# Kernel optimization log

Hardware: AMD Instinct MI355X
Metric: run time of the kernel (lower is better)

The kernel has to match this reference:

```python
import jax, jax.numpy as jnp
import numpy as np
import math

N_HEADS = 16  # matches init_kwargs n_heads


def setup_inputs() -> dict:
    key = jax.random.key(0)
    k1, k2, k3 = jax.random.split(key, 3)
    B, S, D = 8, 1024, 1024
    x = jax.random.normal(k1, (B, S, D), dtype=jnp.float32)
    Wc = jax.random.normal(k2, (D, 3 * D), dtype=jnp.float32) * 0.02
    bc = jnp.zeros((3 * D,), dtype=jnp.float32)
    Wo = jax.random.normal(k3, (D, D), dtype=jnp.float32) * 0.02
    bo = jnp.zeros((D,), dtype=jnp.float32)
    return {"x": x, "Wc": Wc, "bc": bc, "Wo": Wo, "bo": bo}


def reference(x, Wc, bc, Wo, bo):
    B, S, D = x.shape
    H = N_HEADS
    hd = D // H
    qkv = x @ Wc + bc                         # [B,S,3D]
    q, k, v = jnp.split(qkv, 3, axis=2)
    q = q.reshape(B, S, H, hd)
    k = k.reshape(B, S, H, hd)
    v = v.reshape(B, S, H, hd)
    # NOTE: source scales by sqrt(d_size), not sqrt(head_dim)
    scores = jnp.einsum("bqhd,bkhd->bhqk", q, k) / math.sqrt(D)
    # source mask: triu(ones) kept, zeros (k < q) filled with float32 min
    # i.e. attend only to positions k >= q (anti-causal, faithful to source)
    keep = jnp.triu(jnp.ones((S, S), dtype=bool))  # [S,S]
    neg = jnp.finfo(jnp.float32).min
    scores = jnp.where(keep[None, None, :, :], scores, neg)
    attn = jax.nn.softmax(scores, axis=-1)    # [B,H,S,S]; dropout p=0 -> identity
    out = jnp.einsum("bhqk,bkhd->bqhd", attn, v)
    concat = out.reshape(B, S, D)
    return concat @ Wo + bo                   # final dropout p=0 -> identity
```

## Files before the change

kernel.cpp:

```cpp
#include <hip/hip_runtime.h>
#include <stdint.h>

typedef __attribute__((ext_vector_type(8))) short  bf16x8;
typedef __attribute__((ext_vector_type(4))) short  short4v;
typedef __attribute__((ext_vector_type(4))) float  f32x4;
typedef __attribute__((ext_vector_type(4))) float  float4v;

#define VMW(N) asm volatile("s_waitcnt vmcnt(" #N ")" ::: "memory")
#define BAR()  asm volatile("s_barrier" ::: "memory")

__device__ __forceinline__ short f2bf(float f) {
  union { float f; uint32_t u; } c; c.f = f;
  uint32_t u = c.u;
  uint32_t r = (u + 0x7FFFu + ((u >> 16) & 1u)) >> 16;
  return (short)(uint16_t)r;
}

__device__ __forceinline__ short f2bf_hw(float f) {
  return __builtin_bit_cast(short, (__bf16)f);
}

__device__ __forceinline__ void gload_lds16(const void* g, void* l) {
  __builtin_amdgcn_global_load_lds(
      (const __attribute__((address_space(1))) void*)g,
      (__attribute__((address_space(3))) void*)l, 16, 0, 0);
}

__device__ __forceinline__ void transpose_body(
    const float* __restrict__ in, short* __restrict__ out, int R, int C,
    int bx, int by, short (*tile)[65]) {
  int bc = bx * 64, br = by * 64;
  int tc = threadIdx.x & 63, tr = threadIdx.x >> 6;
#pragma unroll
  for (int i = 0; i < 64; i += 4)
    tile[tc][tr + i] = f2bf(in[(size_t)(br + tr + i) * C + bc + tc]);
  __syncthreads();
#pragma unroll
  for (int i = 0; i < 64; i += 4)
    out[(size_t)(bc + tr + i) * R + br + tc] = tile[tr + i][tc];
}

__global__ __launch_bounds__(256) void k_prep(
    const float* __restrict__ x, short* __restrict__ xb, int n4,
    const float* __restrict__ Wc, short* __restrict__ wct,
    const float* __restrict__ Wo, short* __restrict__ wot) {
  __shared__ short tile[64][65];
  const int id = blockIdx.x;
  if (id < 1024) {
    const int stride = 1024 * 256;
    for (int i = id * 256 + threadIdx.x; i < n4; i += stride) {
      float4v v = *(const float4v*)(x + (size_t)i * 4);
      short4v o;
      o.x = f2bf(v.x); o.y = f2bf(v.y); o.z = f2bf(v.z); o.w = f2bf(v.w);
      *(short4v*)(xb + (size_t)i * 4) = o;
    }
  } else if (id < 1024 + 768) {
    int t = id - 1024;
    transpose_body(Wc, wct, 1024, 3072, t % 48, t / 48, tile);
  } else {
    int t = id - 1792;
    transpose_body(Wo, wot, 1024, 1024, t & 15, t >> 4, tile);
  }
}

template <bool F32OUT>
__global__ __launch_bounds__(256) void k_gemm2(
    const short* __restrict__ A, const short* __restrict__ BT,
    const float* __restrict__ bias, void* __restrict__ Cout,
    int M, int N, int K, int nbn) {
  __shared__ short SM[2][2][2][128][32];
  const int tid = threadIdx.x;
  const int w = tid >> 6, l = tid & 63;
  const int fr = l & 15, fg = l >> 4;
  const int wm = w >> 1, wn = w & 1;

  const int q8 = gridDim.x >> 3;
  const int wg = (blockIdx.x & 7) * q8 + (blockIdx.x >> 3);
  const int bm = wg / nbn, bn = wg % nbn;
  const size_t brow = (size_t)bm << 7;
  const int bcol = bn << 7;

  const int NT = K >> 6;

  const int srow = l >> 2;
  const int soct = (l & 3) ^ ((l >> 3) & 3);
  const short* aG = A + (brow + srow) * (size_t)K + soct * 8;
  const short* bG = BT + ((size_t)(bcol + srow)) * K + soct * 8;
  const int slot8 = ((fg ^ ((fr >> 1) & 3)) << 3);

  f32x4 acc[4][4] = {};

#pragma unroll
  for (int s = 0; s < 6; ++s) {
    const int t = s >> 2, tau = s & 3, buf = t & 1, mat = tau & 1, kh = tau >> 1;
    const int kbase = t * 64 + kh * 32;
    const short* g0 = (mat ? bG : aG) + kbase;
#pragma unroll
    for (int j = 0; j < 2; ++j) {
      const int r0 = (w * 2 + j) * 16;
      gload_lds16(g0 + (size_t)r0 * K, (char*)&SM[buf][mat][kh][r0][0]);
    }
  }
  VMW(8);
  BAR();

  int sidx = 6;
  for (int t = 0; t < NT; ++t) {
    const int buf = t & 1;
#pragma unroll
    for (int p = 0; p < 2; ++p) {
      const int kh = p;
#pragma unroll
      for (int s = 0; s < 2; ++s) {
        if (sidx < NT * 4) {
          const int ts = sidx >> 2, tau = sidx & 3;
          const int sb = ts & 1, mat = tau & 1, skh = tau >> 1;
          const int kbase = ts * 64 + skh * 32;
          const short* g0 = (mat ? bG : aG) + kbase;
#pragma unroll
          for (int j = 0; j < 2; ++j) {
            const int r0 = (w * 2 + j) * 16;
            gload_lds16(g0 + (size_t)r0 * K, (char*)&SM[sb][mat][skh][r0][0]);
          }
          ++sidx;
        }
      }
      bf16x8 af[4], bf[4];
#pragma unroll
      for (int m = 0; m < 4; ++m)
        af[m] = *(const bf16x8*)&SM[buf][0][kh][wm * 64 + m * 16 + fr][slot8];
#pragma unroll
      for (int n = 0; n < 4; ++n)
        bf[n] = *(const bf16x8*)&SM[buf][1][kh][wn * 64 + n * 16 + fr][slot8];
      BAR();
      __builtin_amdgcn_s_setprio(1);
#pragma unroll
      for (int m = 0; m < 4; ++m)
#pragma unroll
        for (int n = 0; n < 4; ++n)
          acc[m][n] = __builtin_amdgcn_mfma_f32_16x16x32_bf16(
              af[m], bf[n], acc[m][n], 0, 0, 0);
      __builtin_amdgcn_s_setprio(0);
      if (!(t == NT - 1 && p == 1)) {
        if (t == NT - 1 && p == 0) { VMW(0); }
        else if (t == NT - 2 && p == 1) { VMW(4); }
        else { VMW(8); }
        BAR();
      }
    }
  }

#pragma unroll
  for (int n = 0; n < 4; ++n) {
    const int col = bcol + wn * 64 + n * 16 + fr;
    const float bv = bias[col];
#pragma unroll
    for (int i = 0; i < 4; ++i) {
      const size_t row = brow + (size_t)(wm * 64 + i * 16 + fg * 4);
#pragma unroll
      for (int r = 0; r < 4; ++r) {
        const float v = acc[i][n][r] + bv;
        if (F32OUT)
          ((float*)Cout)[(row + r) * (size_t)N + col] = v;
        else
          ((short*)Cout)[(row + r) * (size_t)N + col] = f2bf(v);
      }
    }
  }
}

__global__ __launch_bounds__(256) void k_attn(
    const short* __restrict__ qkv, short* __restrict__ outc, int Bn, int S) {
  __shared__ short Ks[64][64];
  __shared__ short Vt[64][72];

  const int tid = threadIdx.x;
  const int w = tid >> 6, l = tid & 63;
  const int fr = l & 15, fg = l >> 4;

  const int tq = blockIdx.x >> 7;
  const int bh = blockIdx.x & 127;
  const int h = bh & 15, b = bh >> 4;
  const int q0 = tq << 6;

  const size_t rowbase = (size_t)b * S;
  const int qcol = q0 + w * 16 + fr;

  bf16x8 qf[2];
  {
    const short* qp = qkv + (rowbase + qcol) * 3072 + h * 64 + fg * 8;
    qf[0] = *(const bf16x8*)qp;
    qf[1] = *(const bf16x8*)(qp + 32);
    const float C2 = 0.04508422f;
#pragma unroll
    for (int j = 0; j < 8; ++j) {
      union { float f; uint32_t u; } ca, cb;
      ca.u = ((uint32_t)(uint16_t)qf[0][j]) << 16;
      cb.u = ((uint32_t)(uint16_t)qf[1][j]) << 16;
      qf[0][j] = f2bf_hw(ca.f * C2);
      qf[1][j] = f2bf_hw(cb.f * C2);
    }
  }

  f32x4 o[4] = {};
  f32x4 ol = {};
  const short ONE = (short)0x3F80;
  const bf16x8 vones = {ONE, ONE, ONE, ONE, ONE, ONE, ONE, ONE};

  const short* Kbase = qkv + rowbase * 3072 + 1024 + h * 64;
  const short* Vbase = qkv + rowbase * 3072 + 2048 + h * 64;

  const int r8 = l >> 3, slot = l & 7;
  const int vdb = (tid >> 4) << 2;
  const int vkb = (tid & 15) << 2;

#define STAGE_K(c)                                                             \
  {                                                                            \
    const int k0s = (c) << 6;                                                  \
    _Pragma("unroll") for (int j = 0; j < 2; ++j) {                            \
      int ch = w * 2 + j;                                                      \
      int row = ch * 8 + r8;                                                   \
      int d = (slot ^ (row & 7)) << 3;                                         \
      gload_lds16(Kbase + (size_t)(k0s + row) * 3072 + d,                      \
                  (char*)&Ks[0][0] + ch * 1024);                               \
    }                                                                          \
  }
#define LOAD_V(c)                                                              \
  {                                                                            \
    const int k0s = (c) << 6;                                                  \
    const short* vp = Vbase + (size_t)(k0s + vkb) * 3072 + vdb;                \
    vr[0] = *(const short4v*)(vp);                                             \
    vr[1] = *(const short4v*)(vp + 3072);                                      \
    vr[2] = *(const short4v*)(vp + 2 * 3072);                                  \
    vr[3] = *(const short4v*)(vp + 3 * 3072);                                  \
  }

  const int c0 = tq;
  short4v vr[4];
  STAGE_K(c0);
  LOAD_V(c0);

  for (int c = c0; c < 16; ++c) {
    const int k0 = c << 6;
    VMW(0);
    __syncthreads();

    {
      short4v t0 = {vr[0].x, vr[1].x, vr[2].x, vr[3].x};
      short4v t1 = {vr[0].y, vr[1].y, vr[2].y, vr[3].y};
      short4v t2 = {vr[0].z, vr[1].z, vr[2].z, vr[3].z};
      short4v t3 = {vr[0].w, vr[1].w, vr[2].w, vr[3].w};
      *(short4v*)&Vt[vdb + 0][vkb] = t0;
      *(short4v*)&Vt[vdb + 1][vkb] = t1;
      *(short4v*)&Vt[vdb + 2][vkb] = t2;
      *(short4v*)&Vt[vdb + 3][vkb] = t3;
    }

    f32x4 st[4];
#pragma unroll
    for (int kb = 0; kb < 4; ++kb) {
      f32x4 z = {0.f, 0.f, 0.f, 0.f};
      int row = kb * 16 + fr;
      int sw = row & 7;
      bf16x8 kf0 = *(const bf16x8*)&Ks[row][(fg ^ sw) << 3];
      bf16x8 kf1 = *(const bf16x8*)&Ks[row][((4 + fg) ^ sw) << 3];
      z = __builtin_amdgcn_mfma_f32_16x16x32_bf16(kf0, qf[0], z, 0, 0, 0);
      z = __builtin_amdgcn_mfma_f32_16x16x32_bf16(kf1, qf[1], z, 0, 0, 0);
      st[kb] = z;
    }

    if (c + 1 < 16) LOAD_V(c + 1);

    const bool masked = (c == c0);
#pragma unroll
    for (int kb = 0; kb < 4; ++kb)
#pragma unroll
      for (int r = 0; r < 4; ++r) {
        float e = exp2f(st[kb][r]);
        if (masked) {
          int kg = k0 + kb * 16 + fg * 4 + r;
          e = (kg < qcol) ? 0.0f : e;
        }
        st[kb][r] = e;
      }

    __syncthreads();

    if (c + 1 < 16) STAGE_K(c + 1);

#pragma unroll
    for (int kb2 = 0; kb2 < 2; ++kb2) {
      bf16x8 pa = {f2bf_hw(st[2 * kb2][0]),     f2bf_hw(st[2 * kb2][1]),
                   f2bf_hw(st[2 * kb2][2]),     f2bf_hw(st[2 * kb2][3]),
                   f2bf_hw(st[2 * kb2 + 1][0]), f2bf_hw(st[2 * kb2 + 1][1]),
                   f2bf_hw(st[2 * kb2 + 1][2]), f2bf_hw(st[2 * kb2 + 1][3])};
      ol = __builtin_amdgcn_mfma_f32_16x16x32_bf16(pa, vones, ol, 0, 0, 0);
#pragma unroll
      for (int f = 0; f < 4; ++f) {
        short4v v0 = *(const short4v*)&Vt[f * 16 + fr][kb2 * 32 + fg * 4];
        short4v v1 = *(const short4v*)&Vt[f * 16 + fr][kb2 * 32 + 16 + fg * 4];
        bf16x8 vb = {v0.x, v0.y, v0.z, v0.w, v1.x, v1.y, v1.z, v1.w};
        o[f] = __builtin_amdgcn_mfma_f32_16x16x32_bf16(pa, vb, o[f], 0, 0, 0);
      }
    }
  }
#undef STAGE_K
#undef LOAD_V

#pragma unroll
  for (int r = 0; r < 4; ++r) {
    float inv = 1.0f / ol[r];
    size_t orow = rowbase + (size_t)(q0 + w * 16 + fg * 4 + r);
    short* op = outc + orow * 1024 + h * 64 + fr;
#pragma unroll
    for (int f = 0; f < 4; ++f) op[f * 16] = f2bf(o[f][r] * inv);
  }
}

extern "C" void kernel_launch(void* const* d_in, const int* in_sizes, int n_in,
                              void* d_out, int out_size, void* d_ws,
                              size_t ws_size, hipStream_t stream) {
  const float* x = (const float*)d_in[0];
  const float* Wc = (const float*)d_in[1];
  const float* bc = (const float*)d_in[2];
  const float* Wo = (const float*)d_in[3];
  const float* bo = (const float*)d_in[4];
  float* out = (float*)d_out;

  const int Bn = 8, S = 1024, D = 1024;
  const int M = Bn * S;

  char* ws = (char*)d_ws;
  short* xb  = (short*)(ws);
  short* wct = (short*)(ws + (size_t)16 * 1024 * 1024);
  short* wot = (short*)(ws + (size_t)22 * 1024 * 1024);
  short* qkv = (short*)(ws + (size_t)24 * 1024 * 1024);
  short* cat = (short*)(ws + (size_t)72 * 1024 * 1024);

  k_prep<<<2048, 256, 0, stream>>>(x, xb, M * D / 4, Wc, wct, Wo, wot);
  k_gemm2<false><<<(M / 128) * (3 * D / 128), 256, 0, stream>>>(
      xb, wct, bc, qkv, M, 3 * D, D, 3 * D / 128);
  k_attn<<<16 * 128, 256, 0, stream>>>(qkv, cat, Bn, S);
  k_gemm2<true><<<(M / 128) * (D / 128), 256, 0, stream>>>(
      cat, wot, bo, out, M, D, D, D / 128);
}
```

Baseline: 151.5 us.

## Add 256x256-tile 512-thread GEMM kernel for QKV projection

Adds a new bf16 MFMA GEMM kernel that uses 256x256 output tiles, 8 waves, double-buffered swizzled LDS staging, and interleaves next-tile global->LDS loads with fragment reads and MFMA bursts under raised wave priority. The QKV projection (M=8192, N=3072, K=1024) now uses it in place of the 128x128 kernel. The goal is more arithmetic per loaded byte and less load latency exposed in the largest GEMM. In exchange it needs 128KB of LDS and many accumulator registers per block, which limits occupancy. The grid drops to 384 blocks, which may not balance evenly across the CUs.

```diff
diff --git a/kernel.cpp b/kernel.cpp
--- a/kernel.cpp
+++ b/kernel.cpp
@@ -7,6 +7,7 @@
 typedef __attribute__((ext_vector_type(4))) float  float4v;
 
 #define VMW(N) asm volatile("s_waitcnt vmcnt(" #N ")" ::: "memory")
+#define LKW(N) asm volatile("s_waitcnt lgkmcnt(" #N ")" ::: "memory")
 #define BAR()  asm volatile("s_barrier" ::: "memory")
 
 __device__ __forceinline__ short f2bf(float f) {
@@ -64,6 +65,118 @@
 }
 
 template <bool F32OUT>
+__global__ __launch_bounds__(512)
+__attribute__((amdgpu_waves_per_eu(2, 2))) void k_g256(
+    const short* __restrict__ A, const short* __restrict__ BT,
+    const float* __restrict__ bias, void* __restrict__ Cout,
+    int M, int N, int K, int nbn) {
+  __shared__ short As[2][2][128][64];
+  __shared__ short Bs[2][2][128][64];
+  const int tid = threadIdx.x;
+  const int w = tid >> 6, l = tid & 63;
+  const int fr = l & 15, fg = l >> 4;
+  const int wm = w >> 2, wn = w & 3;
+
+  const int q8 = gridDim.x >> 3;
+  const int wg = (blockIdx.x & 7) * q8 + (blockIdx.x >> 3);
+  const int bm = wg / nbn, bn = wg % nbn;
+  const size_t brow = (size_t)bm << 8;
+  const int bcol = bn << 8;
+  const int NT = K >> 6;
+
+  const int srow = tid >> 3;
+  const int soct = (tid & 7) ^ (srow & 7);
+  const int sx = fr & 7;
+
+  f32x4 acc[8][4] = {};
+
+#define STAGE_A(bufv, halfv, kt)                                               \
+  {                                                                            \
+    _Pragma("unroll") for (int j = 0; j < 2; ++j) {                            \
+      const short* g = A + (brow + (halfv)*128 + j * 64 + srow) * (size_t)K +  \
+                       (kt)*64 + soct * 8;                                     \
+      gload_lds16(g, (char*)&As[bufv][halfv][j * 64 + w * 8][0]);              \
+    }                                                                          \
+  }
+#define STAGE_B(bufv, halfv, kt)                                               \
+  {                                                                            \
+    _Pragma("unroll") for (int j = 0; j < 2; ++j) {                            \
+      const short* g = BT +                                                    \
+                       ((size_t)(bcol + (halfv)*128 + j * 64 + srow)) * K +    \
+                       (kt)*64 + soct * 8;                                     \
+      gload_lds16(g, (char*)&Bs[bufv][halfv][j * 64 + w * 8][0]);              \
+    }                                                                          \
+  }
+
+  STAGE_A(0, 0, 0); STAGE_B(0, 0, 0); STAGE_A(0, 1, 0); STAGE_B(0, 1, 0);
+  VMW(0);
+  BAR();
+
+  const int bhalf = wn >> 1, brow2 = (wn & 1) * 64;
+
+  for (int t = 0; t < NT; ++t) {
+    const int buf = t & 1, nbuf = buf ^ 1;
+    bf16x8 bfr[4][2];
+#pragma unroll
+    for (int p = 0; p < 4; ++p) {
+      bf16x8 afr[2][2];
+#pragma unroll
+      for (int i = 0; i < 2; ++i)
+#pragma unroll
+        for (int kk = 0; kk < 2; ++kk)
+          afr[i][kk] = *(const bf16x8*)
+              &As[buf][wm][(2 * p + i) * 16 + fr][((kk * 4 + fg) ^ sx) * 8];
+      if (p == 0) {
+#pragma unroll
+        for (int nf = 0; nf < 4; ++nf)
+#pragma unroll
+          for (int kk = 0; kk < 2; ++kk)
+            bfr[nf][kk] = *(const bf16x8*)
+                &Bs[buf][bhalf][brow2 + nf * 16 + fr][((kk * 4 + fg) ^ sx) * 8];
+      }
+      if (t + 1 < NT) {
+        if (p == 0) { STAGE_A(nbuf, 0, t + 1); STAGE_B(nbuf, 0, t + 1); }
+        else if (p == 1) { STAGE_A(nbuf, 1, t + 1); STAGE_B(nbuf, 1, t + 1); }
+      }
+      if (p == 0) { LKW(8); }
+      BAR();
+      __builtin_amdgcn_s_setprio(1);
+#pragma unroll
+      for (int i = 0; i < 2; ++i)
+#pragma unroll
+        for (int nf = 0; nf < 4; ++nf)
+#pragma unroll
+          for (int kk = 0; kk < 2; ++kk)
+            acc[2 * p + i][nf] = __builtin_amdgcn_mfma_f32_16x16x32_bf16(
+                afr[i][kk], bfr[nf][kk], acc[2 * p + i][nf], 0, 0, 0);
+      __builtin_amdgcn_s_setprio(0);
+      if (p == 3 && t + 1 < NT) { VMW(0); }
+      BAR();
+    }
+  }
+#undef STAGE_A
+#undef STAGE_B
+
+#pragma unroll
+  for (int nf = 0; nf < 4; ++nf) {
+    const int col = bcol + wn * 64 + nf * 16 + fr;
+    const float bv = bias[col];
+#pragma unroll
+    for (int mf = 0; mf < 8; ++mf) {
+      const size_t row = brow + (size_t)(wm * 128 + mf * 16 + fg * 4);
+#pragma unroll
+      for (int r = 0; r < 4; ++r) {
+        const float v = acc[mf][nf][r] + bv;
+        if (F32OUT)
+          ((float*)Cout)[(row + r) * (size_t)N + col] = v;
+        else
+          ((short*)Cout)[(row + r) * (size_t)N + col] = f2bf(v);
+      }
+    }
+  }
+}
+
+template <bool F32OUT>
 __global__ __launch_bounds__(256) void k_gemm2(
     const short* __restrict__ A, const short* __restrict__ BT,
     const float* __restrict__ bias, void* __restrict__ Cout,
@@ -338,8 +451,8 @@
   short* cat = (short*)(ws + (size_t)72 * 1024 * 1024);
 
   k_prep<<<2048, 256, 0, stream>>>(x, xb, M * D / 4, Wc, wct, Wo, wot);
-  k_gemm2<false><<<(M / 128) * (3 * D / 128), 256, 0, stream>>>(
-      xb, wct, bc, qkv, M, 3 * D, D, 3 * D / 128);
+  k_g256<false><<<(M / 256) * (3 * D / 256), 512, 0, stream>>>(
+      xb, wct, bc, qkv, M, 3 * D, D, 3 * D / 256);
   k_attn<<<16 * 128, 256, 0, stream>>>(qkv, cat, Bn, S);
   k_gemm2<true><<<(M / 128) * (D / 128), 256, 0, stream>>>(
       cat, wot, bo, out, M, D, D, D / 128);
```

After: 158.6 us. 1.05x slower.
